# Kernel tuning notes

Measured on AMD Instinct MI355X. Metric: run time of the kernel, lower is better.

The kernel has to match this reference:

```python
import jax, jax.numpy as jnp
import numpy as np

N_NODES = 4096
F_UAV = 64
N_OBS = N_NODES * F_UAV + 256  # 262400
H = 1024
N_ACT = 64
N_EDGES = 65536


def setup_inputs() -> dict:
    key = jax.random.key(0)
    ks = jax.random.split(key, 13)
    s = lambda fan_in: 1.0 / np.sqrt(fan_in)
    return {
        "node_x": jax.random.normal(ks[0], (N_NODES, F_UAV), jnp.float32),
        "flat_obs": jax.random.normal(ks[1], (N_OBS,), jnp.float32),
        "gcn_w": jax.random.normal(ks[2], (F_UAV, F_UAV), jnp.float32) * s(F_UAV),
        "gcn_b": jnp.zeros((F_UAV,), jnp.float32),
        "w1": jax.random.normal(ks[3], (N_OBS, H), jnp.float32) * s(N_OBS),
        "b1": jnp.zeros((H,), jnp.float32),
        "w2": jax.random.normal(ks[4], (H, H), jnp.float32) * s(H),
        "b2": jnp.zeros((H,), jnp.float32),
        "wv": jax.random.normal(ks[5], (H, 1), jnp.float32) * s(H),
        "bv": jnp.zeros((1,), jnp.float32),
        "wa": jax.random.normal(ks[6], (H, N_ACT), jnp.float32) * s(H),
        "ba": jnp.zeros((N_ACT,), jnp.float32),
        "edge_index": jax.random.randint(ks[7], (2, N_EDGES), 0, N_NODES, jnp.int64),
    }


def _gcn_conv(x, edge_index, w, b):
    n = x.shape[0]
    loops = jnp.arange(n, dtype=edge_index.dtype)
    src = jnp.concatenate([edge_index[0], loops])
    dst = jnp.concatenate([edge_index[1], loops])
    deg = jax.ops.segment_sum(jnp.ones_like(dst, dtype=x.dtype), dst, num_segments=n)
    dinv = jax.lax.rsqrt(deg)  # deg >= 1 thanks to self-loops
    norm = dinv[src] * dinv[dst]          # [E+N]
    h = x @ w                              # [N, F]
    msg = h[src] * norm[:, None]           # gather + scale
    out = jax.ops.segment_sum(msg, dst, num_segments=n)  # scatter-add
    return out + b


def reference(node_x, flat_obs, gcn_w, gcn_b, w1, b1, w2, b2, wv, bv, wa, ba, edge_index):
    y_uav = _gcn_conv(node_x, edge_index, gcn_w, gcn_b).reshape(-1)  # flatten
    x = jnp.concatenate([y_uav, flat_obs[y_uav.shape[0]:]], axis=0)  # [N_OBS]
    y = jax.nn.relu(x @ w1 + b1)
    y = jax.nn.relu(y @ w2 + b2)
    value = y @ wv + bv                    # [1]
    adv = y @ wa + ba                      # [N_ACT]
    return value + adv - jnp.mean(adv, keepdims=True)
```

## Files before the change

kernel.cpp:

```cpp
#include <hip/hip_runtime.h>

#define N_NODES 4096
#define F_UAV 64
#define NOBS 262400
#define GCN_FLAT (N_NODES * F_UAV)
#define HDIM 1024
#define N_ACT 64
#define N_EDGES 65536

typedef float f32x4 __attribute__((ext_vector_type(4)));
typedef float f32x2 __attribute__((ext_vector_type(2)));

#define MV1_GRID 2048
#define MV1_BIGN 256
#define MV1_BIG 129
#define MV1_SMALL 128

#define OFF_X      0
#define OFF_H      262400
#define OFF_DINV   (OFF_H + GCN_FLAT)
#define OFF_DEG    (OFF_DINV + N_NODES)
#define OFF_BASE   (OFF_DEG + N_NODES)
#define OFF_CUR    (OFF_BASE + N_NODES)
#define OFF_SSRC   (OFF_CUR + N_NODES)
#define OFF_P1     (OFF_SSRC + N_EDGES)
#define OFF_Q1T    (OFF_P1 + 2048*1024)
#define OFF_P2     (OFF_Q1T + 1024*128)
#define OFF_Q2T    (OFF_P2 + 256*1024)

__global__ __launch_bounds__(256) void k_gcn_h(const float* __restrict__ nx,
                                               const float* __restrict__ w,
                                               const int* __restrict__ dst,
                                               float* __restrict__ h,
                                               int* __restrict__ deg) {
    __shared__ float sw[F_UAV * F_UAV];
    __shared__ float sx4[256];
    int tid = threadIdx.x;
    for (int i = tid; i < F_UAV * F_UAV; i += 256) sw[i] = w[i];
    sx4[tid] = nx[blockIdx.x * 256 + tid];
    if (blockIdx.x < 256) atomicAdd(&deg[dst[blockIdx.x * 256 + tid]], 1);
    __syncthreads();
    int r = tid >> 6, j = tid & 63;
    float acc = 0.f;
#pragma unroll
    for (int k = 0; k < F_UAV; ++k) acc += sx4[r * 64 + k] * sw[k * F_UAV + j];
    h[blockIdx.x * 256 + r * 64 + j] = acc;
}

__global__ __launch_bounds__(1024) void k_prefix(const int* __restrict__ deg,
                                                 int* __restrict__ base,
                                                 int* __restrict__ cursor,
                                                 float* __restrict__ dinv,
                                                 const float* __restrict__ obs,
                                                 float* __restrict__ x) {
    __shared__ int ssum[1024];
    int t = threadIdx.x;
    int d0 = deg[4 * t], d1 = deg[4 * t + 1], d2 = deg[4 * t + 2], d3 = deg[4 * t + 3];
    int local = d0 + d1 + d2 + d3;
    ssum[t] = local;
    __syncthreads();
    for (int off = 1; off < 1024; off <<= 1) {
        int v = (t >= off) ? ssum[t - off] : 0;
        __syncthreads();
        ssum[t] += v;
        __syncthreads();
    }
    int excl = ssum[t] - local;
    int b0 = excl, b1 = b0 + d0, b2 = b1 + d1, b3 = b2 + d2;
    base[4 * t] = b0;     cursor[4 * t] = b0;
    base[4 * t + 1] = b1; cursor[4 * t + 1] = b1;
    base[4 * t + 2] = b2; cursor[4 * t + 2] = b2;
    base[4 * t + 3] = b3; cursor[4 * t + 3] = b3;
    dinv[4 * t]     = rsqrtf((float)(d0 + 1));
    dinv[4 * t + 1] = rsqrtf((float)(d1 + 1));
    dinv[4 * t + 2] = rsqrtf((float)(d2 + 1));
    dinv[4 * t + 3] = rsqrtf((float)(d3 + 1));
    if (t < NOBS - GCN_FLAT) x[GCN_FLAT + t] = obs[GCN_FLAT + t];
}

__global__ void k_place(const int* __restrict__ src, const int* __restrict__ dst,
                        int* __restrict__ cursor, int* __restrict__ ssrc) {
    int e = blockIdx.x * 256 + threadIdx.x;
    if (e < N_EDGES) {
        int slot = atomicAdd(&cursor[dst[e]], 1);
        ssrc[slot] = src[e];
    }
}

__global__ __launch_bounds__(256) void k_gather(const int* __restrict__ base,
                                                const int* __restrict__ deg,
                                                const int* __restrict__ ssrc,
                                                const float* __restrict__ h,
                                                const float* __restrict__ dinv,
                                                const float* __restrict__ gb,
                                                float* __restrict__ x) {
    int tid = threadIdx.x;
    int n = blockIdx.x * 4 + (tid >> 6);
    int j = tid & 63;
    int lo = base[n], cnt = deg[n];
    int end = lo + cnt;
    float acc0 = 0.f, acc1 = 0.f;
    int i = lo;
    for (; i + 1 < end; i += 2) {
        int s0 = ssrc[i], s1 = ssrc[i + 1];
        acc0 += h[s0 * 64 + j] * dinv[s0];
        acc1 += h[s1 * 64 + j] * dinv[s1];
    }
    if (i < end) {
        int s = ssrc[i];
        acc0 += h[s * 64 + j] * dinv[s];
    }
    float dn = dinv[n];
    x[n * 64 + j] = (acc0 + acc1) * dn + h[n * 64 + j] * dn * dn + gb[j];
}

__global__ __launch_bounds__(256) void k_matvec(const float* __restrict__ x,
                                                const float* __restrict__ W,
                                                float* __restrict__ part,
                                                int big_n, int big_sz, int small_sz) {
    __shared__ float sx[132];
    int tid = threadIdx.x;
    int b = blockIdx.x;
    int k0 = (b < big_n) ? b * big_sz : big_n * big_sz + (b - big_n) * small_sz;
    int cnt = (b < big_n) ? big_sz : small_sz;
    for (int i = tid; i < cnt; i += 256) sx[i] = x[k0 + i];
    __syncthreads();
    f32x4 acc = {0.f, 0.f, 0.f, 0.f};
    const f32x4* Wr = ((const f32x4*)W) + (size_t)k0 * (HDIM / 4) + tid;
    int kk = cnt & ~7;
    int k = 0;
    for (; k < kk; k += 8) {
#pragma unroll
        for (int u = 0; u < 8; ++u) {
            float xv = sx[k + u];
            f32x4 w = __builtin_nontemporal_load(&Wr[(size_t)(k + u) * (HDIM / 4)]);
            acc += xv * w;
        }
    }
    for (; k < cnt; ++k) acc += sx[k] * __builtin_nontemporal_load(&Wr[(size_t)k * (HDIM / 4)]);
    ((f32x4*)(part + (size_t)b * HDIM))[tid] = acc;
}

template <int NSEG>
__global__ __launch_bounds__(256) void k_sum16T(const float* __restrict__ part,
                                                float* __restrict__ qT) {
    int t = threadIdx.x, s = blockIdx.x;
    const f32x4* p = ((const f32x4*)part) + (size_t)s * 16 * (HDIM / 4) + t;
    f32x4 acc = {0.f, 0.f, 0.f, 0.f};
#pragma unroll
    for (int r = 0; r < 16; ++r) acc += p[(size_t)r * (HDIM / 4)];
#pragma unroll
    for (int u = 0; u < 4; ++u) qT[(size_t)(4 * t + u) * NSEG + s] = acc[u];
}

__global__ __launch_bounds__(256) void k_fin_mv2(const float* __restrict__ q1T,
                                                 const float* __restrict__ b1,
                                                 const float* __restrict__ w2,
                                                 float* __restrict__ p2) {
    __shared__ float s_y[4];
    int t = threadIdx.x, b = blockIdx.x;
    int w = t >> 6, l = t & 63;
    int j = 4 * b + w;
    f32x2 v = *(const f32x2*)&q1T[(size_t)j * 128 + 2 * l];
    float sm = v.x + v.y;
    for (int off = 32; off; off >>= 1) sm += __shfl_xor(sm, off);
    if (l == 0) s_y[w] = fmaxf(b1[j] + sm, 0.f);
    __syncthreads();
    f32x4 acc = {0.f, 0.f, 0.f, 0.f};
    const f32x4* Wr = ((const f32x4*)w2) + (size_t)(4 * b) * (HDIM / 4) + t;
#pragma unroll
    for (int i = 0; i < 4; ++i) acc += s_y[i] * Wr[(size_t)i * (HDIM / 4)];
    ((f32x4*)(p2 + (size_t)b * HDIM))[t] = acc;
}

__global__ __launch_bounds__(1024) void k_heads_f(const float* __restrict__ q2T,
                                                  const float* __restrict__ b2,
                                                  const float* __restrict__ wv,
                                                  const float* __restrict__ bv,
                                                  const float* __restrict__ wa,
                                                  const float* __restrict__ ba,
                                                  float* __restrict__ out) {
    __shared__ float y2s[1024];
    __shared__ float s_adv[16][64];
    __shared__ float s_pv[1024];
    int t = threadIdx.x;
    float acc = b2[t];
#pragma unroll
    for (int s = 0; s < 16; ++s) acc += q2T[t * 16 + s];
    float y = fmaxf(acc, 0.f);
    y2s[t] = y;
    s_pv[t] = y * wv[t];
    __syncthreads();
    int g = t >> 6, a = t & 63;
    float pa = 0.f;
#pragma unroll 4
    for (int kk = 0; kk < 64; ++kk) pa += y2s[g * 64 + kk] * wa[(g * 64 + kk) * 64 + a];
    s_adv[g][a] = pa;
    __syncthreads();
    if (t < 64) {
        float adv = ba[a];
#pragma unroll
        for (int gg = 0; gg < 16; ++gg) adv += s_adv[gg][a];
        float v = 0.f;
#pragma unroll
        for (int i = 0; i < 16; ++i) v += s_pv[a + 64 * i];
        for (int off = 32; off; off >>= 1) v += __shfl_xor(v, off);
        float m = adv;
        for (int off = 32; off; off >>= 1) m += __shfl_xor(m, off);
        m *= (1.f / 64.f);
        out[a] = (v + bv[0]) + adv - m;
    }
}

extern "C" void kernel_launch(void* const* d_in, const int* in_sizes, int n_in,
                              void* d_out, int out_size, void* d_ws, size_t ws_size,
                              hipStream_t stream) {
    const float* node_x   = (const float*)d_in[0];
    const float* flat_obs = (const float*)d_in[1];
    const float* gcn_w    = (const float*)d_in[2];
    const float* gcn_b    = (const float*)d_in[3];
    const float* w1       = (const float*)d_in[4];
    const float* b1       = (const float*)d_in[5];
    const float* w2       = (const float*)d_in[6];
    const float* b2       = (const float*)d_in[7];
    const float* wv       = (const float*)d_in[8];
    const float* bv       = (const float*)d_in[9];
    const float* wa       = (const float*)d_in[10];
    const float* ba       = (const float*)d_in[11];
    const int*   ei       = (const int*)d_in[12];
    const int* src = ei;
    const int* dst = ei + N_EDGES;

    float* ws   = (float*)d_ws;
    float* x    = ws + OFF_X;
    float* h    = ws + OFF_H;
    float* dinv = ws + OFF_DINV;
    int*   deg  = (int*)(ws + OFF_DEG);
    int*   base = (int*)(ws + OFF_BASE);
    int*   cur  = (int*)(ws + OFF_CUR);
    int*   ssrc = (int*)(ws + OFF_SSRC);
    float* p1   = ws + OFF_P1;
    float* q1T  = ws + OFF_Q1T;
    float* p2   = ws + OFF_P2;
    float* q2T  = ws + OFF_Q2T;
    float* out  = (float*)d_out;

    hipMemsetAsync(deg, 0, N_NODES * sizeof(int), stream);
    k_gcn_h<<<N_NODES / 4, 256, 0, stream>>>(node_x, gcn_w, dst, h, deg);
    k_prefix<<<1, 1024, 0, stream>>>(deg, base, cur, dinv, flat_obs, x);
    k_place<<<N_EDGES / 256, 256, 0, stream>>>(src, dst, cur, ssrc);
    k_gather<<<N_NODES / 4, 256, 0, stream>>>(base, deg, ssrc, h, dinv, gcn_b, x);

    k_matvec<<<MV1_GRID, 256, 0, stream>>>(x, w1, p1, MV1_BIGN, MV1_BIG, MV1_SMALL);
    k_sum16T<128><<<128, 256, 0, stream>>>(p1, q1T);
    k_fin_mv2<<<256, 256, 0, stream>>>(q1T, b1, w2, p2);
    k_sum16T<16><<<16, 256, 0, stream>>>(p2, q2T);
    k_heads_f<<<1, 1024, 0, stream>>>(q2T, b2, wv, bv, wa, ba, out);
}
```

Baseline: 230.1 us.

## Replace CSR-sort GCN with atomic edge scatter and merge final reduction into heads

The GCN aggregation no longer builds a CSR ordering through prefix-sum, placement and gather kernels. One kernel now computes the edge normalisation from degrees on the fly and atomically adds each message into x, covering self-loops, bias and the flat_obs tail too. The second matvec is regrouped to 16 rows per block, 64 blocks, so the separate sum kernel is dropped and k_heads_f reduces the 64 partials directly. This cuts several launches and a serial single-block scan, at the cost of float atomics into x (non-deterministic summation order) and a wider memset.

```diff
diff --git a/kernel.cpp b/kernel.cpp
--- a/kernel.cpp
+++ b/kernel.cpp
@@ -17,16 +17,11 @@
 #define MV1_SMALL 128
 
 #define OFF_X      0
-#define OFF_H      262400
-#define OFF_DINV   (OFF_H + GCN_FLAT)
-#define OFF_DEG    (OFF_DINV + N_NODES)
-#define OFF_BASE   (OFF_DEG + N_NODES)
-#define OFF_CUR    (OFF_BASE + N_NODES)
-#define OFF_SSRC   (OFF_CUR + N_NODES)
-#define OFF_P1     (OFF_SSRC + N_EDGES)
+#define OFF_DEG    262400
+#define OFF_H      (OFF_DEG + N_NODES)
+#define OFF_P1     (OFF_H + GCN_FLAT)
 #define OFF_Q1T    (OFF_P1 + 2048*1024)
 #define OFF_P2     (OFF_Q1T + 1024*128)
-#define OFF_Q2T    (OFF_P2 + 256*1024)
 
 __global__ __launch_bounds__(256) void k_gcn_h(const float* __restrict__ nx,
                                                const float* __restrict__ w,
@@ -47,71 +42,33 @@
     h[blockIdx.x * 256 + r * 64 + j] = acc;
 }
 
-__global__ __launch_bounds__(1024) void k_prefix(const int* __restrict__ deg,
-                                                 int* __restrict__ base,
-                                                 int* __restrict__ cursor,
-                                                 float* __restrict__ dinv,
-                                                 const float* __restrict__ obs,
-                                                 float* __restrict__ x) {
-    __shared__ int ssum[1024];
-    int t = threadIdx.x;
-    int d0 = deg[4 * t], d1 = deg[4 * t + 1], d2 = deg[4 * t + 2], d3 = deg[4 * t + 3];
-    int local = d0 + d1 + d2 + d3;
-    ssum[t] = local;
-    __syncthreads();
-    for (int off = 1; off < 1024; off <<= 1) {
-        int v = (t >= off) ? ssum[t - off] : 0;
-        __syncthreads();
-        ssum[t] += v;
-        __syncthreads();
-    }
-    int excl = ssum[t] - local;
-    int b0 = excl, b1 = b0 + d0, b2 = b1 + d1, b3 = b2 + d2;
-    base[4 * t] = b0;     cursor[4 * t] = b0;
-    base[4 * t + 1] = b1; cursor[4 * t + 1] = b1;
-    base[4 * t + 2] = b2; cursor[4 * t + 2] = b2;
-    base[4 * t + 3] = b3; cursor[4 * t + 3] = b3;
-    dinv[4 * t]     = rsqrtf((float)(d0 + 1));
-    dinv[4 * t + 1] = rsqrtf((float)(d1 + 1));
-    dinv[4 * t + 2] = rsqrtf((float)(d2 + 1));
-    dinv[4 * t + 3] = rsqrtf((float)(d3 + 1));
-    if (t < NOBS - GCN_FLAT) x[GCN_FLAT + t] = obs[GCN_FLAT + t];
-}
-
-__global__ void k_place(const int* __restrict__ src, const int* __restrict__ dst,
-                        int* __restrict__ cursor, int* __restrict__ ssrc) {
-    int e = blockIdx.x * 256 + threadIdx.x;
-    if (e < N_EDGES) {
-        int slot = atomicAdd(&cursor[dst[e]], 1);
-        ssrc[slot] = src[e];
-    }
-}
-
-__global__ __launch_bounds__(256) void k_gather(const int* __restrict__ base,
-                                                const int* __restrict__ deg,
-                                                const int* __restrict__ ssrc,
-                                                const float* __restrict__ h,
-                                                const float* __restrict__ dinv,
-                                                const float* __restrict__ gb,
-                                                float* __restrict__ x) {
+__global__ __launch_bounds__(256) void k_scatter_all(const int* __restrict__ src,
+                                                     const int* __restrict__ dst,
+                                                     const int* __restrict__ deg,
+                                                     const float* __restrict__ h,
+                                                     const float* __restrict__ gb,
+                                                     const float* __restrict__ obs,
+                                                     float* __restrict__ x) {
+    int b = blockIdx.x;
     int tid = threadIdx.x;
-    int n = blockIdx.x * 4 + (tid >> 6);
-    int j = tid & 63;
-    int lo = base[n], cnt = deg[n];
-    int end = lo + cnt;
-    float acc0 = 0.f, acc1 = 0.f;
-    int i = lo;
-    for (; i + 1 < end; i += 2) {
-        int s0 = ssrc[i], s1 = ssrc[i + 1];
-        acc0 += h[s0 * 64 + j] * dinv[s0];
-        acc1 += h[s1 * 64 + j] * dinv[s1];
-    }
-    if (i < end) {
-        int s = ssrc[i];
-        acc0 += h[s * 64 + j] * dinv[s];
-    }
-    float dn = dinv[n];
-    x[n * 64 + j] = (acc0 + acc1) * dn + h[n * 64 + j] * dn * dn + gb[j];
+    if (b < N_EDGES / 4) {
+        int e = b * 4 + (tid >> 6);
+        int j = tid & 63;
+        int s = src[e], d = dst[e];
+        float norm = rsqrtf((deg[s] + 1.0f) * (deg[d] + 1.0f));
+        atomicAdd(&x[d * 64 + j], h[s * 64 + j] * norm);
+    } else if (b < N_EDGES / 4 + 256) {
+        int base = (b - N_EDGES / 4) * 1024 + tid * 4;
+        int n = base >> 6;
+        float dinv2 = 1.0f / (float)(deg[n] + 1);
+#pragma unroll
+        for (int u = 0; u < 4; ++u) {
+            int idx = base + u;
+            atomicAdd(&x[idx], h[idx] * dinv2 + gb[idx & 63]);
+        }
+    } else {
+        if (tid < NOBS - GCN_FLAT) x[GCN_FLAT + tid] = obs[GCN_FLAT + tid];
+    }
 }
 
 __global__ __launch_bounds__(256) void k_matvec(const float* __restrict__ x,
@@ -157,23 +114,26 @@
                                                  const float* __restrict__ b1,
                                                  const float* __restrict__ w2,
                                                  float* __restrict__ p2) {
-    __shared__ float s_y[4];
+    __shared__ float s_y[16];
     int t = threadIdx.x, b = blockIdx.x;
     int w = t >> 6, l = t & 63;
-    int j = 4 * b + w;
-    f32x2 v = *(const f32x2*)&q1T[(size_t)j * 128 + 2 * l];
-    float sm = v.x + v.y;
-    for (int off = 32; off; off >>= 1) sm += __shfl_xor(sm, off);
-    if (l == 0) s_y[w] = fmaxf(b1[j] + sm, 0.f);
+#pragma unroll
+    for (int rr = 0; rr < 4; ++rr) {
+        int j = 16 * b + 4 * w + rr;
+        f32x2 v = *(const f32x2*)&q1T[(size_t)j * 128 + 2 * l];
+        float sm = v.x + v.y;
+        for (int off = 32; off; off >>= 1) sm += __shfl_xor(sm, off);
+        if (l == 0) s_y[4 * w + rr] = fmaxf(b1[j] + sm, 0.f);
+    }
     __syncthreads();
     f32x4 acc = {0.f, 0.f, 0.f, 0.f};
-    const f32x4* Wr = ((const f32x4*)w2) + (size_t)(4 * b) * (HDIM / 4) + t;
-#pragma unroll
-    for (int i = 0; i < 4; ++i) acc += s_y[i] * Wr[(size_t)i * (HDIM / 4)];
+    const f32x4* Wr = ((const f32x4*)w2) + (size_t)(16 * b) * (HDIM / 4) + t;
+#pragma unroll
+    for (int i = 0; i < 16; ++i) acc += s_y[i] * Wr[(size_t)i * (HDIM / 4)];
     ((f32x4*)(p2 + (size_t)b * HDIM))[t] = acc;
 }
 
-__global__ __launch_bounds__(1024) void k_heads_f(const float* __restrict__ q2T,
+__global__ __launch_bounds__(1024) void k_heads_f(const float* __restrict__ p2,
                                                   const float* __restrict__ b2,
                                                   const float* __restrict__ wv,
                                                   const float* __restrict__ bv,
@@ -185,8 +145,8 @@
     __shared__ float s_pv[1024];
     int t = threadIdx.x;
     float acc = b2[t];
-#pragma unroll
-    for (int s = 0; s < 16; ++s) acc += q2T[t * 16 + s];
+#pragma unroll 8
+    for (int s = 0; s < 64; ++s) acc += p2[s * HDIM + t];
     float y = fmaxf(acc, 0.f);
     y2s[t] = y;
     s_pv[t] = y * wv[t];
@@ -233,27 +193,20 @@
 
     float* ws   = (float*)d_ws;
     float* x    = ws + OFF_X;
+    int*   deg  = (int*)(ws + OFF_DEG);
     float* h    = ws + OFF_H;
-    float* dinv = ws + OFF_DINV;
-    int*   deg  = (int*)(ws + OFF_DEG);
-    int*   base = (int*)(ws + OFF_BASE);
-    int*   cur  = (int*)(ws + OFF_CUR);
-    int*   ssrc = (int*)(ws + OFF_SSRC);
     float* p1   = ws + OFF_P1;
     float* q1T  = ws + OFF_Q1T;
     float* p2   = ws + OFF_P2;
-    float* q2T  = ws + OFF_Q2T;
     float* out  = (float*)d_out;
 
-    hipMemsetAsync(deg, 0, N_NODES * sizeof(int), stream);
-    k_gcn_h<<<N_NODES / 4, 256, 0, stream>>>(node_x, gcn_w, dst, h, deg);
-    k_prefix<<<1, 1024, 0, stream>>>(deg, base, cur, dinv, flat_obs, x);
-    k_place<<<N_EDGES / 256, 256, 0, stream>>>(src, dst, cur, ssrc);
-    k_gather<<<N_NODES / 4, 256, 0, stream>>>(base, deg, ssrc, h, dinv, gcn_b, x);
+    hipMemsetAsync(x, 0, (NOBS + N_NODES) * sizeof(float), stream);
+    k_gcn_h<<<GCN_FLAT / 256, 256, 0, stream>>>(node_x, gcn_w, dst, h, deg);
+    k_scatter_all<<<N_EDGES / 4 + 256 + 1, 256, 0, stream>>>(src, dst, deg, h,
+                                                             gcn_b, flat_obs, x);
 
     k_matvec<<<MV1_GRID, 256, 0, stream>>>(x, w1, p1, MV1_BIGN, MV1_BIG, MV1_SMALL);
     k_sum16T<128><<<128, 256, 0, stream>>>(p1, q1T);
-    k_fin_mv2<<<256, 256, 0, stream>>>(q1T, b1, w2, p2);
-    k_sum16T<16><<<16, 256, 0, stream>>>(p2, q2T);
-    k_heads_f<<<1, 1024, 0, stream>>>(q2T, b2, wv, bv, wa, ba, out);
-}
+    k_fin_mv2<<<64, 256, 0, stream>>>(q1T, b1, w2, p2);
+    k_heads_f<<<1, 1024, 0, stream>>>(p2, b2, wv, bv, wa, ba, out);
+}
```

After: 231.7 us. Within noise of the previous version (+0.7%).
